# Kernel tuning notes

Hardware: AMD Instinct MI355X
Metric: run time of the kernel (lower is better)

The kernel has to match this reference:

```python
import jax, jax.numpy as jnp
import numpy as np

NUM_HEADS = 16


def setup_inputs() -> dict:
    key = jax.random.key(0)
    ks = jax.random.split(key, 5)
    B, N, C = 4, 2048, 1024
    x = jax.random.normal(ks[0], (B, N, C), dtype=jnp.float32)
    mask = jax.random.randint(ks[1], (B, N), 0, 2, dtype=jnp.int32)
    W_qkv = jax.random.normal(ks[2], (C, 3 * C), dtype=jnp.float32) * (C ** -0.5)
    W_proj = jax.random.normal(ks[3], (C, C), dtype=jnp.float32) * (C ** -0.5)
    b_proj = jnp.zeros((C,), dtype=jnp.float32)
    return {"x": x, "mask": mask, "W_qkv": W_qkv, "W_proj": W_proj, "b_proj": b_proj}


def reference(x, mask, W_qkv, W_proj, b_proj):
    B, N, C = x.shape
    H = NUM_HEADS
    hd = C // H
    scale = hd ** -0.5
    # qkv projection -> [3, B, H, N, hd]
    qkv = (x @ W_qkv).reshape(B, N, 3, H, hd).transpose(2, 0, 3, 1, 4)
    q, k, v = qkv[0], qkv[1], qkv[2]
    attn = jnp.einsum('bhqd,bhkd->bhqk', q, k) * scale  # [B,H,N,N]
    add_mask = (mask[:, None, None, :] != 1).astype(jnp.float32) * -10000.0
    attn = jax.nn.softmax(attn + add_mask, axis=-1)
    out = jnp.einsum('bhqk,bhkd->bhqd', attn, v)  # [B,H,N,hd]
    out = out.transpose(0, 2, 1, 3).reshape(B, N, C)
    return out @ W_proj + b_proj
```

## Files before the change

### kernel.cpp

```cpp
#include <hip/hip_runtime.h>

typedef unsigned short u16;
typedef unsigned int u32;
typedef unsigned long long u64;
typedef __attribute__((ext_vector_type(8))) short short8;
typedef __attribute__((ext_vector_type(4))) float f32x4;

#define QSCALE 0.18033688f

__device__ __forceinline__ u16 f2bf(float f) {
  u32 u = __builtin_bit_cast(u32, f);
  u += 0x7fffu + ((u >> 16) & 1u);
  return (u16)(u >> 16);
}

__device__ __forceinline__ float fexp2(float x) {
#if __has_builtin(__builtin_amdgcn_exp2f)
  return __builtin_amdgcn_exp2f(x);
#else
  return exp2f(x);
#endif
}

__device__ __forceinline__ void glds16(u16* lds, const u16* g) {
  __builtin_amdgcn_global_load_lds(
      (const __attribute__((address_space(1))) u32*)g,
      (__attribute__((address_space(3))) u32*)lds, 16, 0, 0);
}

#define MFMA(a, b, c) __builtin_amdgcn_mfma_f32_16x16x32_bf16((a), (b), (c), 0, 0, 0)


__global__ __launch_bounds__(256) void prep(const float* __restrict__ x,
                                            const int* __restrict__ mask,
                                            const float* __restrict__ Wqkv,
                                            const float* __restrict__ Wproj,
                                            u16* __restrict__ xb,
                                            u16* __restrict__ wqkvt,
                                            u16* __restrict__ wprojt,
                                            int* __restrict__ s2t,
                                            int* __restrict__ nkbuf) {
  __shared__ float tile[64][65];
  __shared__ int wtot[4];
  __shared__ int wbase[5];
  const int bid = blockIdx.x, t = threadIdx.x;

  if (bid < 8192) {
    int i = bid * 256 + t;
    float4 v = ((const float4*)x)[i];
    union { u16 s[4]; u64 ll; } u;
    u.s[0] = f2bf(v.x); u.s[1] = f2bf(v.y); u.s[2] = f2bf(v.z); u.s[3] = f2bf(v.w);
    ((u64*)xb)[i] = u.ll;
    return;
  }
  if (bid < 9216) {
    const float* Wm; u16* Wt; int Cc, bj, bi;
    if (bid < 8960) { int tt = bid - 8192; Wm = Wqkv;  Wt = wqkvt;  Cc = 3072; bj = tt % 48; bi = tt / 48; }
    else            { int tt = bid - 8960; Wm = Wproj; Wt = wprojt; Cc = 1024; bj = tt & 15; bi = tt >> 4; }
    const int r = t >> 4, c4 = (t & 15) << 2;
    for (int rr = r; rr < 64; rr += 16) {
      float4 v = *(const float4*)&Wm[(size_t)(bi * 64 + rr) * Cc + bj * 64 + c4];
      tile[rr][c4] = v.x; tile[rr][c4 + 1] = v.y; tile[rr][c4 + 2] = v.z; tile[rr][c4 + 3] = v.w;
    }
    __syncthreads();
    for (int rr = r; rr < 64; rr += 16) {
      union { u16 s[4]; u64 ll; } u;
      u.s[0] = f2bf(tile[c4][rr]);
      u.s[1] = f2bf(tile[c4 + 1][rr]);
      u.s[2] = f2bf(tile[c4 + 2][rr]);
      u.s[3] = f2bf(tile[c4 + 3][rr]);
      *(u64*)&Wt[(size_t)(bj * 64 + rr) * 1024 + bi * 64 + c4] = u.ll;
    }
    return;
  }
  const int b = bid - 9216;
  const int lane = t & 63, w = t >> 6;
  int m8[8], c = 0;
  #pragma unroll
  for (int j = 0; j < 8; j++) {
    m8[j] = (mask[b * 2048 + t * 8 + j] == 1);
    c += m8[j];
  }
  int incl = c;
  #pragma unroll
  for (int off = 1; off < 64; off <<= 1) {
    int v = __shfl_up(incl, off);
    if (lane >= off) incl += v;
  }
  if (lane == 63) wtot[w] = incl;
  __syncthreads();
  if (t == 0) {
    int s = 0;
    for (int i = 0; i < 4; i++) { wbase[i] = s; s += wtot[i]; }
    wbase[4] = s;
  }
  __syncthreads();
  const int nk = wbase[4];
  int urun = wbase[w] + incl - c;
  #pragma unroll
  for (int j = 0; j < 8; j++) {
    int tok = t * 8 + j;
    int slot = m8[j] ? urun : nk + (tok - urun);
    s2t[b * 2048 + slot] = b * 2048 + tok;
    urun += m8[j];
  }
  if (t == 0) nkbuf[b] = nk;
}

__global__ __launch_bounds__(256, 4) void gemm_fused(const u16* __restrict__ xb,
                                                     const u16* __restrict__ wqkvt,
                                                     const int* __restrict__ s2t,
                                                     const int* __restrict__ nkbuf,
                                                     u16* __restrict__ qbuf,
                                                     u16* __restrict__ kc,
                                                     u16* __restrict__ vtc) {
  __shared__ u16 Asm[128 * 64];
  __shared__ u16 Bsm[128 * 64];
  const int bid = blockIdx.x;
  const int role = bid >> 9;
  const int sub = bid & 511;
  const int tid = threadIdx.x, lane = tid & 63, w = tid >> 6;
  const int quad = lane >> 4, l15 = lane & 15;
  const int wm = (w >> 1) * 64, wn = (w & 1) * 64;
  const int srow = lane >> 3;
  const int gcc = ((lane & 7) ^ srow) * 8;
  const int rx8 = (l15 & 7);

  int m0, n0;
  if (role == 2) { m0 = (sub >> 6) * 128; n0 = (sub & 63) * 128; }
  else           { m0 = (sub & 63) * 128; n0 = (sub >> 6) * 128; }
  if (role == 1 && (m0 & 2047) >= nkbuf[m0 >> 11]) return;
  if (role == 2 && (n0 & 2047) >= nkbuf[n0 >> 11]) return;

  int arow[4], brow[4];
  #pragma unroll
  for (int c = 0; c < 4; ++c) {
    int rit = (w * 4 + c) * 8 + srow;
    if (role == 0)      { arow[c] = m0 + rit;            brow[c] = n0 + rit; }
    else if (role == 1) { arow[c] = s2t[m0 + rit];       brow[c] = 1024 + n0 + rit; }
    else                { arow[c] = 2048 + m0 + rit;     brow[c] = s2t[n0 + rit]; }
  }
  const u16 *Asrc = (role == 2) ? wqkvt : xb;
  const u16 *Bsrc = (role == 2) ? xb : wqkvt;

  f32x4 acc[4][4];
  #pragma unroll
  for (int i = 0; i < 4; i++)
    #pragma unroll
    for (int j = 0; j < 4; j++)
      #pragma unroll
      for (int r = 0; r < 4; r++) acc[i][j][r] = 0.f;

  for (int kt = 0; kt < 1024; kt += 64) {
    __syncthreads();
    #pragma unroll
    for (int c = 0; c < 4; ++c) {
      int chunk = w * 4 + c;
      glds16(&Asm[chunk * 512], &Asrc[(size_t)arow[c] * 1024 + kt + gcc]);
      glds16(&Bsm[chunk * 512], &Bsrc[(size_t)brow[c] * 1024 + kt + gcc]);
    }
    __syncthreads();
    #pragma unroll
    for (int ks = 0; ks < 2; ++ks) {
      int pc = ((ks * 4 + quad) ^ rx8) * 8;
      short8 av[4], bv[4];
      #pragma unroll
      for (int i = 0; i < 4; i++)
        av[i] = *(const short8*)&Asm[(wm + i * 16 + l15) * 64 + pc];
      #pragma unroll
      for (int j = 0; j < 4; j++)
        bv[j] = *(const short8*)&Bsm[(wn + j * 16 + l15) * 64 + pc];
      #pragma unroll
      for (int i = 0; i < 4; i++)
        #pragma unroll
        for (int j = 0; j < 4; j++)
          acc[i][j] = MFMA(av[i], bv[j], acc[i][j]);
    }
  }

  if (role == 2) {
    #pragma unroll
    for (int j = 0; j < 4; j++) {
      int col = n0 + wn + j * 16 + l15;
      int bb = col >> 11, sl = col & 2047;
      #pragma unroll
      for (int i = 0; i < 4; i++)
        #pragma unroll
        for (int r = 0; r < 4; r++) {
          int row = m0 + wm + i * 16 + quad * 4 + r;
          vtc[(size_t)(bb * 1024 + row) * 2048 + sl] = f2bf(acc[i][j][r]);
        }
    }
  } else {
    u16* dst = (role == 0) ? qbuf : kc;
    const float sc = (role == 0) ? QSCALE : 1.f;
    #pragma unroll
    for (int i = 0; i < 4; i++)
      #pragma unroll
      for (int j = 0; j < 4; j++) {
        int col = n0 + wn + j * 16 + l15;
        #pragma unroll
        for (int r = 0; r < 4; r++) {
          int row = m0 + wm + i * 16 + quad * 4 + r;
          dst[(size_t)row * 1024 + col] = f2bf(acc[i][j][r] * sc);
        }
      }
  }
}

__global__ __launch_bounds__(256, 2) void attn_kernel(const u16* __restrict__ q,
                                                      const u16* __restrict__ kc,
                                                      const u16* __restrict__ vtc,
                                                      const int* __restrict__ nkbuf,
                                                      u16* __restrict__ ao) {
  __shared__ u16 Ksm[2][2][64 * 64];
  __shared__ u16 Vsm[2][2][64 * 64];
  const int h = blockIdx.x, b = blockIdx.y, qt = blockIdx.z;
  const int tid = threadIdx.x, lane = tid & 63, w = tid >> 6;
  const int quad = lane >> 4, l15 = lane & 15;
  const int q0 = qt * 256 + w * 64;
  const int srow = lane >> 3;
  const int gcc = ((lane & 7) ^ srow) * 8;
  const int rx8 = (l15 & 7);
  const int nk = nkbuf[b];
  const int nt2 = (nk + 127) >> 7;
  const int quad8 = quad * 8;

  int vrow[2], prow[2];
  #pragma unroll
  for (int c = 0; c < 2; ++c) {
    int row = (w * 2 + c) * 8 + srow;
    vrow[c] = row;
    prow[c] = ((row >> 4) & 1) * 32 + ((row >> 2) & 3) * 8 + ((row >> 5) & 1) * 4 + (row & 3);
  }

  short8 ones;
  #pragma unroll
  for (int z = 0; z < 8; z++) ones[z] = (short)0x3F80;

  short8 qf[4][2];
  #pragma unroll
  for (int i = 0; i < 4; i++)
    #pragma unroll
    for (int ks = 0; ks < 2; ks++)
      qf[i][ks] = *(const short8*)&q[(size_t)(b * 2048 + q0 + i * 16 + l15) * 1024 +
                                     h * 64 + ks * 32 + quad * 8];

  f32x4 o[4][4], osum[4];
  #pragma unroll
  for (int i = 0; i < 4; i++) {
    #pragma unroll
    for (int r = 0; r < 4; r++) osum[i][r] = 0.f;
    #pragma unroll
    for (int jd = 0; jd < 4; jd++)
      #pragma unroll
      for (int r = 0; r < 4; r++) o[i][jd][r] = 0.f;
  }

#define STAGEKV(pb_, t_) {                                                             \
    const int k0s = (t_) * 128;                                                        \
    _Pragma("unroll") for (int c = 0; c < 2; ++c) {                                    \
      int chunk = w * 2 + c;                                                           \
      glds16(&Ksm[pb_][0][chunk * 512],                                                \
             &kc[(size_t)(b * 2048 + k0s + prow[c]) * 1024 + h * 64 + gcc]);           \
      glds16(&Vsm[pb_][0][chunk * 512],                                                \
             &vtc[(size_t)(b * 1024 + h * 64 + vrow[c]) * 2048 + k0s + gcc]);          \
      glds16(&Ksm[pb_][1][chunk * 512],                                                \
             &kc[(size_t)(b * 2048 + k0s + 64 + prow[c]) * 1024 + h * 64 + gcc]);      \
      glds16(&Vsm[pb_][1][chunk * 512],                                                \
             &vtc[(size_t)(b * 1024 + h * 64 + vrow[c]) * 2048 + k0s + 64 + gcc]);     \
    }                                                                                  \
  }

#define SUBTILE(pb_, st_, kbase_)                                                      \
  {                                                                                    \
    f32x4 s[4][4];                                                                     \
    _Pragma("unroll") for (int j = 0; j < 4; j++)                                      \
      _Pragma("unroll") for (int i = 0; i < 4; i++)                                    \
        _Pragma("unroll") for (int r = 0; r < 4; r++) s[j][i][r] = 0.f;                \
    _Pragma("unroll") for (int ks = 0; ks < 2; ks++) {                                 \
      int pc = ((ks * 4 + quad) ^ rx8) * 8;                                            \
      short8 kf[4];                                                                    \
      _Pragma("unroll") for (int j = 0; j < 4; j++)                                    \
        kf[j] = *(const short8*)&Ksm[pb_][st_][(j * 16 + l15) * 64 + pc];              \
      __builtin_amdgcn_s_setprio(1);                                                   \
      _Pragma("unroll") for (int j = 0; j < 4; j++)                                    \
        _Pragma("unroll") for (int i = 0; i < 4; i++)                                  \
          s[j][i] = MFMA(kf[j], qf[i][ks], s[j][i]);                                   \
      __builtin_amdgcn_s_setprio(0);                                                   \
    }                                                                                  \
    const bool tail = ((kbase_) + 64 > nk);                                            \
    short8 pf[4][2];                                                                   \
    _Pragma("unroll") for (int i = 0; i < 4; i++) {                                    \
      float p[4][4];                                                                   \
      if (!tail) {                                                                     \
        _Pragma("unroll") for (int j = 0; j < 4; j++)                                  \
          _Pragma("unroll") for (int r = 0; r < 4; r++)                                \
            p[j][r] = fexp2(s[j][i][r]);                                               \
      } else {                                                                         \
        _Pragma("unroll") for (int j = 0; j < 4; j++)                                  \
          _Pragma("unroll") for (int r = 0; r < 4; r++) {                              \
            int slot = (kbase_) + (j & 1) * 32 + quad8 + (j >> 1) * 4 + r;             \
            float e = fexp2(s[j][i][r]);                                               \
            p[j][r] = (slot < nk) ? e : 0.f;                                           \
          }                                                                            \
      }                                                                                \
      _Pragma("unroll") for (int ks = 0; ks < 2; ks++) {                               \
        union { u32 u[4]; short8 v; } pk;                                              \
        u32 a0 = __builtin_bit_cast(u32, p[ks][0]) + 0x8000u;                          \
        u32 a1 = __builtin_bit_cast(u32, p[ks][1]) + 0x8000u;                          \
        u32 a2 = __builtin_bit_cast(u32, p[ks][2]) + 0x8000u;                          \
        u32 a3 = __builtin_bit_cast(u32, p[ks][3]) + 0x8000u;                          \
        u32 b0 = __builtin_bit_cast(u32, p[ks + 2][0]) + 0x8000u;                      \
        u32 b1 = __builtin_bit_cast(u32, p[ks + 2][1]) + 0x8000u;                      \
        u32 b2 = __builtin_bit_cast(u32, p[ks + 2][2]) + 0x8000u;                      \
        u32 b3 = __builtin_bit_cast(u32, p[ks + 2][3]) + 0x8000u;                      \
        pk.u[0] = __builtin_amdgcn_perm(a1, a0, 0x07060302u);                          \
        pk.u[1] = __builtin_amdgcn_perm(a3, a2, 0x07060302u);                          \
        pk.u[2] = __builtin_amdgcn_perm(b1, b0, 0x07060302u);                          \
        pk.u[3] = __builtin_amdgcn_perm(b3, b2, 0x07060302u);                          \
        pf[i][ks] = pk.v;                                                              \
      }                                                                                \
    }                                                                                  \
    _Pragma("unroll") for (int ks = 0; ks < 2; ks++) {                                 \
      int pcv = ((ks * 4 + quad) ^ rx8) * 8;                                           \
      short8 vf[4];                                                                    \
      _Pragma("unroll") for (int jd = 0; jd < 4; jd++)                                 \
        vf[jd] = *(const short8*)&Vsm[pb_][st_][(jd * 16 + l15) * 64 + pcv];           \
      __builtin_amdgcn_s_setprio(1);                                                   \
      _Pragma("unroll") for (int i = 0; i < 4; i++) {                                  \
        osum[i] = MFMA(pf[i][ks], ones, osum[i]);                                      \
        _Pragma("unroll") for (int jd = 0; jd < 4; jd++)                               \
          o[i][jd] = MFMA(pf[i][ks], vf[jd], o[i][jd]);                                \
      }                                                                                \
      __builtin_amdgcn_s_setprio(0);                                                   \
    }                                                                                  \
  }

  STAGEKV(0, 0)
  __syncthreads();
  for (int t = 0; t < nt2; ++t) {
    const int k0 = t * 128;
    const int pb = t & 1;
    if (t + 1 < nt2) STAGEKV(pb ^ 1, t + 1)
    SUBTILE(pb, 0, k0)
    if (k0 + 64 < nk) SUBTILE(pb, 1, k0 + 64)
    __syncthreads();
  }
#undef SUBTILE
#undef STAGEKV

  #pragma unroll
  for (int i = 0; i < 4; i++)
    #pragma unroll
    for (int r = 0; r < 4; r++) {
      float inv = 1.f / osum[i][r];
      size_t row = (size_t)(b * 2048 + q0 + i * 16 + quad * 4 + r);
      #pragma unroll
      for (int jd = 0; jd < 4; jd++)
        ao[row * 1024 + h * 64 + jd * 16 + l15] = f2bf(o[i][jd][r] * inv);
    }
}

__global__ __launch_bounds__(256, 3) void gemm_proj(const u16* __restrict__ A,
                                                    const u16* __restrict__ Bt,
                                                    const float* __restrict__ bias,
                                                    float* __restrict__ out) {
  __shared__ u16 Asm[2][128 * 64];
  __shared__ u16 Bsm[2][128 * 64];
  const int tid = threadIdx.x, lane = tid & 63, w = tid >> 6;
  const int quad = lane >> 4, l15 = lane & 15;
  const int m0 = (blockIdx.x & 63) * 128, n0 = (blockIdx.x >> 6) * 128;
  const int wm = (w >> 1) * 64, wn = (w & 1) * 64;
  const int srow = lane >> 3;
  const int gcc = ((lane & 7) ^ srow) * 8;
  const int rx8 = (l15 & 7);
  f32x4 acc[4][4];
  #pragma unroll
  for (int i = 0; i < 4; i++)
    #pragma unroll
    for (int j = 0; j < 4; j++)
      #pragma unroll
      for (int r = 0; r < 4; r++) acc[i][j][r] = 0.f;

#define STAGEP(pb_, kt_) {                                                             \
    _Pragma("unroll") for (int c = 0; c < 4; ++c) {                                    \
      int chunk = w * 4 + c;                                                           \
      int row = chunk * 8 + srow;                                                      \
      glds16(&Asm[pb_][chunk * 512], &A[(size_t)(m0 + row) * 1024 + (kt_) + gcc]);     \
      glds16(&Bsm[pb_][chunk * 512], &Bt[(size_t)(n0 + row) * 1024 + (kt_) + gcc]);    \
    }                                                                                  \
  }

  STAGEP(0, 0)
  __syncthreads();
  for (int kt = 0, t = 0; kt < 1024; kt += 64, ++t) {
    const int pb = t & 1;
    if (kt + 64 < 1024) STAGEP(pb ^ 1, kt + 64)
    #pragma unroll
    for (int ks = 0; ks < 2; ++ks) {
      int pc = ((ks * 4 + quad) ^ rx8) * 8;
      short8 av[4], bv[4];
      #pragma unroll
      for (int i = 0; i < 4; i++)
        av[i] = *(const short8*)&Asm[pb][(wm + i * 16 + l15) * 64 + pc];
      #pragma unroll
      for (int j = 0; j < 4; j++)
        bv[j] = *(const short8*)&Bsm[pb][(wn + j * 16 + l15) * 64 + pc];
      #pragma unroll
      for (int i = 0; i < 4; i++)
        #pragma unroll
        for (int j = 0; j < 4; j++)
          acc[i][j] = MFMA(av[i], bv[j], acc[i][j]);
    }
    __syncthreads();
  }
#undef STAGEP

  #pragma unroll
  for (int j = 0; j < 4; j++) {
    int col = n0 + wn + j * 16 + l15;
    float bj = bias[col];
    #pragma unroll
    for (int i = 0; i < 4; i++) {
      #pragma unroll
      for (int r = 0; r < 4; r++) {
        int row = m0 + wm + i * 16 + quad * 4 + r;
        out[(size_t)row * 1024 + col] = acc[i][j][r] + bj;
      }
    }
  }
}

extern "C" void kernel_launch(void* const* d_in, const int* in_sizes, int n_in,
                              void* d_out, int out_size, void* d_ws, size_t ws_size,
                              hipStream_t stream) {
  (void)in_sizes; (void)n_in; (void)out_size; (void)ws_size;
  const float* x     = (const float*)d_in[0];
  const int*   mask  = (const int*)d_in[1];
  const float* Wqkv  = (const float*)d_in[2];
  const float* Wproj = (const float*)d_in[3];
  const float* bproj = (const float*)d_in[4];
  float* out = (float*)d_out;
  char* ws = (char*)d_ws;

  size_t off = 0;
  u16* xb     = (u16*)(ws + off); off += 8192ull * 1024 * 2;
  u16* wqkvt  = (u16*)(ws + off); off += 3072ull * 1024 * 2;
  u16* wprojt = (u16*)(ws + off); off += 1024ull * 1024 * 2;
  u16* qbuf   = (u16*)(ws + off); off += 8192ull * 1024 * 2;
  u16* kcbuf  = (u16*)(ws + off); off += 4096ull * 2048 * 2;
  u16* vtcbuf = (u16*)(ws + off); off += 4096ull * 2048 * 2;
  int* s2t    = (int*)(ws + off); off += 8192ull * 4;
  int* nkbuf  = (int*)(ws + off); off += 4 * 4;
  u16* aobuf  = xb;

  prep<<<9220, 256, 0, stream>>>(x, mask, Wqkv, Wproj, xb, wqkvt, wprojt, s2t, nkbuf);
  gemm_fused<<<1536, 256, 0, stream>>>(xb, wqkvt, s2t, nkbuf, qbuf, kcbuf, vtcbuf);
  attn_kernel<<<dim3(16, 4, 8), 256, 0, stream>>>(qbuf, kcbuf, vtcbuf, nkbuf, aobuf);
  gemm_proj<<<512, 256, 0, stream>>>(aobuf, wprojt, bproj, out);
}
```

Before: 206.4 us.

## Rewrite QKV GEMM as 256x256 tile with double-buffered LDS pipeline

The fused QKV projection GEMM moves from 128x128 tiles with 4 waves to 256x256 tiles with 8 waves. It uses double-buffered LDS, staging the next K-tile's A and B loads interleaved with MFMA phases, and adds raw s_barrier plus s_setprio around the MFMA bursts. The aim is to raise operand reuse per LDS byte and hide global-to-LDS latency behind compute, replacing the old load-sync-compute loop. The costs are 128KB of LDS per block, a larger accumulator register footprint, and coarser early-exit granularity for the masked K/V roles.

```diff
diff --git a/kernel.cpp b/kernel.cpp
--- a/kernel.cpp
+++ b/kernel.cpp
@@ -29,6 +29,7 @@
 }
 
 #define MFMA(a, b, c) __builtin_amdgcn_mfma_f32_16x16x32_bf16((a), (b), (c), 0, 0, 0)
+#define SBAR() asm volatile("s_barrier" ::: "memory")
 
 
 __global__ __launch_bounds__(256) void prep(const float* __restrict__ x,
@@ -107,102 +108,138 @@
   if (t == 0) nkbuf[b] = nk;
 }
 
-__global__ __launch_bounds__(256, 4) void gemm_fused(const u16* __restrict__ xb,
+__global__ __launch_bounds__(512, 2) void gemm_fused(const u16* __restrict__ xb,
                                                      const u16* __restrict__ wqkvt,
                                                      const int* __restrict__ s2t,
                                                      const int* __restrict__ nkbuf,
                                                      u16* __restrict__ qbuf,
                                                      u16* __restrict__ kc,
                                                      u16* __restrict__ vtc) {
-  __shared__ u16 Asm[128 * 64];
-  __shared__ u16 Bsm[128 * 64];
+  __shared__ u16 ldsf[2 * 32768];
   const int bid = blockIdx.x;
-  const int role = bid >> 9;
-  const int sub = bid & 511;
+  const int role = bid >> 7;
+  const int sub = bid & 127;
   const int tid = threadIdx.x, lane = tid & 63, w = tid >> 6;
   const int quad = lane >> 4, l15 = lane & 15;
-  const int wm = (w >> 1) * 64, wn = (w & 1) * 64;
-  const int srow = lane >> 3;
-  const int gcc = ((lane & 7) ^ srow) * 8;
-  const int rx8 = (l15 & 7);
+  const int wm = (w >> 2) * 128, wn = (w & 3) * 64;
+  const int rx8 = l15 & 7;
+  const int srow6 = tid >> 3;
+  const int sgc = ((tid & 7) ^ (srow6 & 7)) * 8;
 
   int m0, n0;
-  if (role == 2) { m0 = (sub >> 6) * 128; n0 = (sub & 63) * 128; }
-  else           { m0 = (sub & 63) * 128; n0 = (sub >> 6) * 128; }
+  if (role == 2) { m0 = (sub >> 5) * 256; n0 = (sub & 31) * 256; }
+  else           { m0 = (sub & 31) * 256; n0 = (sub >> 5) * 256; }
   if (role == 1 && (m0 & 2047) >= nkbuf[m0 >> 11]) return;
   if (role == 2 && (n0 & 2047) >= nkbuf[n0 >> 11]) return;
 
-  int arow[4], brow[4];
-  #pragma unroll
-  for (int c = 0; c < 4; ++c) {
-    int rit = (w * 4 + c) * 8 + srow;
-    if (role == 0)      { arow[c] = m0 + rit;            brow[c] = n0 + rit; }
-    else if (role == 1) { arow[c] = s2t[m0 + rit];       brow[c] = 1024 + n0 + rit; }
-    else                { arow[c] = 2048 + m0 + rit;     brow[c] = s2t[n0 + rit]; }
-  }
-  const u16 *Asrc = (role == 2) ? wqkvt : xb;
-  const u16 *Bsrc = (role == 2) ? xb : wqkvt;
-
-  f32x4 acc[4][4];
-  #pragma unroll
-  for (int i = 0; i < 4; i++)
+  int aro[4], bro[4];
+  #pragma unroll
+  for (int q = 0; q < 4; ++q) {
+    int r = q * 64 + srow6;
+    if (role == 0)      { aro[q] = m0 + r;         bro[q] = n0 + r; }
+    else if (role == 1) { aro[q] = s2t[m0 + r];    bro[q] = 1024 + n0 + r; }
+    else                { aro[q] = 2048 + m0 + r;  bro[q] = s2t[n0 + r]; }
+  }
+  const u16* Asrc = (role == 2) ? wqkvt : xb;
+  const u16* Bsrc = (role == 2) ? xb : wqkvt;
+
+#define ABUF(T) (ldsf + (((T) & 1) * 32768))
+#define BBUF(T) (ldsf + (((T) & 1) * 32768 + 16384))
+#define STG_A(H, T) { \
+  glds16(ABUF(T) + ((H) * 128 + w * 8) * 64,      &Asrc[(size_t)aro[(H) * 2]     * 1024 + (T) * 64 + sgc]); \
+  glds16(ABUF(T) + ((H) * 128 + 64 + w * 8) * 64, &Asrc[(size_t)aro[(H) * 2 + 1] * 1024 + (T) * 64 + sgc]); }
+#define STG_B(H, T) { \
+  glds16(BBUF(T) + ((H) * 128 + w * 8) * 64,      &Bsrc[(size_t)bro[(H) * 2]     * 1024 + (T) * 64 + sgc]); \
+  glds16(BBUF(T) + ((H) * 128 + 64 + w * 8) * 64, &Bsrc[(size_t)bro[(H) * 2 + 1] * 1024 + (T) * 64 + sgc]); }
+
+#define LDA8(MH) \
+  _Pragma("unroll") for (int ii = 0; ii < 4; ++ii) \
+    _Pragma("unroll") for (int ks = 0; ks < 2; ++ks) \
+      av[ii][ks] = *(const short8*)&LA[(wm + (MH) * 64 + ii * 16 + l15) * 64 + (((ks * 4 + quad) ^ rx8) * 8)];
+#define LDB4(NH) \
+  _Pragma("unroll") for (int jj = 0; jj < 2; ++jj) \
+    _Pragma("unroll") for (int ks = 0; ks < 2; ++ks) \
+      bv[jj][ks] = *(const short8*)&LB[(wn + (NH) * 32 + jj * 16 + l15) * 64 + (((ks * 4 + quad) ^ rx8) * 8)];
+#define MM16(MH, NH) \
+  __builtin_amdgcn_s_setprio(1); \
+  _Pragma("unroll") for (int ks = 0; ks < 2; ++ks) \
+    _Pragma("unroll") for (int ii = 0; ii < 4; ++ii) \
+      _Pragma("unroll") for (int jj = 0; jj < 2; ++jj) \
+        acc[(MH) * 4 + ii][(NH) * 2 + jj] = MFMA(av[ii][ks], bv[jj][ks], acc[(MH) * 4 + ii][(NH) * 2 + jj]); \
+  __builtin_amdgcn_s_setprio(0);
+
+  f32x4 acc[8][4];
+  #pragma unroll
+  for (int i = 0; i < 8; i++)
     #pragma unroll
     for (int j = 0; j < 4; j++)
       #pragma unroll
       for (int r = 0; r < 4; r++) acc[i][j][r] = 0.f;
 
-  for (int kt = 0; kt < 1024; kt += 64) {
-    __syncthreads();
-    #pragma unroll
-    for (int c = 0; c < 4; ++c) {
-      int chunk = w * 4 + c;
-      glds16(&Asm[chunk * 512], &Asrc[(size_t)arow[c] * 1024 + kt + gcc]);
-      glds16(&Bsm[chunk * 512], &Bsrc[(size_t)brow[c] * 1024 + kt + gcc]);
-    }
-    __syncthreads();
-    #pragma unroll
-    for (int ks = 0; ks < 2; ++ks) {
-      int pc = ((ks * 4 + quad) ^ rx8) * 8;
-      short8 av[4], bv[4];
-      #pragma unroll
-      for (int i = 0; i < 4; i++)
-        av[i] = *(const short8*)&Asm[(wm + i * 16 + l15) * 64 + pc];
-      #pragma unroll
-      for (int j = 0; j < 4; j++)
-        bv[j] = *(const short8*)&Bsm[(wn + j * 16 + l15) * 64 + pc];
-      #pragma unroll
-      for (int i = 0; i < 4; i++)
-        #pragma unroll
-        for (int j = 0; j < 4; j++)
-          acc[i][j] = MFMA(av[i], bv[j], acc[i][j]);
-    }
-  }
+  STG_A(0, 0) STG_A(1, 0) STG_B(0, 0) STG_B(1, 0)
+  STG_B(0, 1) STG_B(1, 1)
+  asm volatile("s_waitcnt vmcnt(4)" ::: "memory");
+  SBAR();
+
+  for (int T = 0; T < 16; ++T) {
+    const u16* LA = ABUF(T);
+    const u16* LB = BBUF(T);
+    short8 av[4][2], bv[2][2];
+    LDA8(0) LDB4(0)
+    if (T + 1 < 16) { STG_A(0, T + 1) }
+    SBAR();
+    MM16(0, 0)
+    SBAR();
+    LDA8(1)
+    if (T + 1 < 16) { STG_A(1, T + 1) }
+    SBAR();
+    MM16(1, 0)
+    SBAR();
+    LDB4(1)
+    SBAR();
+    MM16(1, 1)
+    SBAR();
+    LDA8(0)
+    if (T + 2 < 16) { STG_B(0, T + 2) STG_B(1, T + 2) }
+    SBAR();
+    MM16(0, 1)
+    if (T + 2 < 16)      { asm volatile("s_waitcnt vmcnt(4)" ::: "memory"); }
+    else if (T + 1 < 16) { asm volatile("s_waitcnt vmcnt(0)" ::: "memory"); }
+    SBAR();
+  }
+#undef ABUF
+#undef BBUF
+#undef STG_A
+#undef STG_B
+#undef LDA8
+#undef LDB4
+#undef MM16
 
   if (role == 2) {
     #pragma unroll
-    for (int j = 0; j < 4; j++) {
-      int col = n0 + wn + j * 16 + l15;
+    for (int nj = 0; nj < 4; nj++) {
+      int col = n0 + wn + nj * 16 + l15;
       int bb = col >> 11, sl = col & 2047;
       #pragma unroll
-      for (int i = 0; i < 4; i++)
+      for (int mi = 0; mi < 8; mi++)
         #pragma unroll
         for (int r = 0; r < 4; r++) {
-          int row = m0 + wm + i * 16 + quad * 4 + r;
-          vtc[(size_t)(bb * 1024 + row) * 2048 + sl] = f2bf(acc[i][j][r]);
+          int row = m0 + wm + mi * 16 + quad * 4 + r;
+          vtc[(size_t)(bb * 1024 + row) * 2048 + sl] = f2bf(acc[mi][nj][r]);
         }
     }
   } else {
     u16* dst = (role == 0) ? qbuf : kc;
     const float sc = (role == 0) ? QSCALE : 1.f;
     #pragma unroll
-    for (int i = 0; i < 4; i++)
-      #pragma unroll
-      for (int j = 0; j < 4; j++) {
-        int col = n0 + wn + j * 16 + l15;
+    for (int mi = 0; mi < 8; mi++)
+      #pragma unroll
+      for (int nj = 0; nj < 4; nj++) {
+        int col = n0 + wn + nj * 16 + l15;
         #pragma unroll
         for (int r = 0; r < 4; r++) {
-          int row = m0 + wm + i * 16 + quad * 4 + r;
-          dst[(size_t)row * 1024 + col] = f2bf(acc[i][j][r] * sc);
+          int row = m0 + wm + mi * 16 + quad * 4 + r;
+          dst[(size_t)row * 1024 + col] = f2bf(acc[mi][nj][r] * sc);
         }
       }
   }
@@ -456,7 +493,7 @@
   u16* aobuf  = xb;
 
   prep<<<9220, 256, 0, stream>>>(x, mask, Wqkv, Wproj, xb, wqkvt, wprojt, s2t, nkbuf);
-  gemm_fused<<<1536, 256, 0, stream>>>(xb, wqkvt, s2t, nkbuf, qbuf, kcbuf, vtcbuf);
+  gemm_fused<<<384, 512, 0, stream>>>(xb, wqkvt, s2t, nkbuf, qbuf, kcbuf, vtcbuf);
   attn_kernel<<<dim3(16, 4, 8), 256, 0, stream>>>(qbuf, kcbuf, vtcbuf, nkbuf, aobuf);
   gemm_proj<<<512, 256, 0, stream>>>(aobuf, wprojt, bproj, out);
 }
```

Measured after the change: 224.4 us. 1.09x slower.

## Double attention block to 8 waves sharing each staged K/V tile

Applied to the files above, without the earlier changes.

The attention kernel now uses 512 threads (8 waves) per block, with each block covering 512 query rows instead of 256, so the grid's z dimension halves. Each K/V tile staged in LDS is reused by twice as many waves, and each wave issues half as many global-to-LDS copies. The cost is half as many blocks (256), which may leave some of the GPU's compute units idle. Removing the min-blocks hint from launch bounds may also change register allocation and occupancy.

```diff
diff --git a/kernel.cpp b/kernel.cpp
--- a/kernel.cpp
+++ b/kernel.cpp
@@ -208,17 +208,17 @@
   }
 }
 
-__global__ __launch_bounds__(256, 2) void attn_kernel(const u16* __restrict__ q,
-                                                      const u16* __restrict__ kc,
-                                                      const u16* __restrict__ vtc,
-                                                      const int* __restrict__ nkbuf,
-                                                      u16* __restrict__ ao) {
+__global__ __launch_bounds__(512) void attn_kernel(const u16* __restrict__ q,
+                                                   const u16* __restrict__ kc,
+                                                   const u16* __restrict__ vtc,
+                                                   const int* __restrict__ nkbuf,
+                                                   u16* __restrict__ ao) {
   __shared__ u16 Ksm[2][2][64 * 64];
   __shared__ u16 Vsm[2][2][64 * 64];
   const int h = blockIdx.x, b = blockIdx.y, qt = blockIdx.z;
   const int tid = threadIdx.x, lane = tid & 63, w = tid >> 6;
   const int quad = lane >> 4, l15 = lane & 15;
-  const int q0 = qt * 256 + w * 64;
+  const int q0 = qt * 512 + w * 64;
   const int srow = lane >> 3;
   const int gcc = ((lane & 7) ^ srow) * 8;
   const int rx8 = (l15 & 7);
@@ -226,13 +226,10 @@
   const int nt2 = (nk + 127) >> 7;
   const int quad8 = quad * 8;
 
-  int vrow[2], prow[2];
-  #pragma unroll
-  for (int c = 0; c < 2; ++c) {
-    int row = (w * 2 + c) * 8 + srow;
-    vrow[c] = row;
-    prow[c] = ((row >> 4) & 1) * 32 + ((row >> 2) & 3) * 8 + ((row >> 5) & 1) * 4 + (row & 3);
-  }
+  const int strow = w * 8 + srow;
+  const int vrow = strow;
+  const int prow = ((strow >> 4) & 1) * 32 + ((strow >> 2) & 3) * 8 +
+                   ((strow >> 5) & 1) * 4 + (strow & 3);
 
   short8 ones;
   #pragma unroll
@@ -259,17 +256,14 @@
 
 #define STAGEKV(pb_, t_) {                                                             \
     const int k0s = (t_) * 128;                                                        \
-    _Pragma("unroll") for (int c = 0; c < 2; ++c) {                                    \
-      int chunk = w * 2 + c;                                                           \
-      glds16(&Ksm[pb_][0][chunk * 512],                                                \
-             &kc[(size_t)(b * 2048 + k0s + prow[c]) * 1024 + h * 64 + gcc]);           \
-      glds16(&Vsm[pb_][0][chunk * 512],                                                \
-             &vtc[(size_t)(b * 1024 + h * 64 + vrow[c]) * 2048 + k0s + gcc]);          \
-      glds16(&Ksm[pb_][1][chunk * 512],                                                \
-             &kc[(size_t)(b * 2048 + k0s + 64 + prow[c]) * 1024 + h * 64 + gcc]);      \
-      glds16(&Vsm[pb_][1][chunk * 512],                                                \
-             &vtc[(size_t)(b * 1024 + h * 64 + vrow[c]) * 2048 + k0s + 64 + gcc]);     \
-    }                                                                                  \
+    glds16(&Ksm[pb_][0][w * 512],                                                      \
+           &kc[(size_t)(b * 2048 + k0s + prow) * 1024 + h * 64 + gcc]);                \
+    glds16(&Vsm[pb_][0][w * 512],                                                      \
+           &vtc[(size_t)(b * 1024 + h * 64 + vrow) * 2048 + k0s + gcc]);               \
+    glds16(&Ksm[pb_][1][w * 512],                                                      \
+           &kc[(size_t)(b * 2048 + k0s + 64 + prow) * 1024 + h * 64 + gcc]);           \
+    glds16(&Vsm[pb_][1][w * 512],                                                      \
+           &vtc[(size_t)(b * 1024 + h * 64 + vrow) * 2048 + k0s + 64 + gcc]);          \
   }
 
 #define SUBTILE(pb_, st_, kbase_)                                                      \
@@ -457,6 +451,6 @@
 
   prep<<<9220, 256, 0, stream>>>(x, mask, Wqkv, Wproj, xb, wqkvt, wprojt, s2t, nkbuf);
   gemm_fused<<<1536, 256, 0, stream>>>(xb, wqkvt, s2t, nkbuf, qbuf, kcbuf, vtcbuf);
-  attn_kernel<<<dim3(16, 4, 8), 256, 0, stream>>>(qbuf, kcbuf, vtcbuf, nkbuf, aobuf);
+  attn_kernel<<<dim3(16, 4, 4), 512, 0, stream>>>(qbuf, kcbuf, vtcbuf, nkbuf, aobuf);
   gemm_proj<<<512, 256, 0, stream>>>(aobuf, wprojt, bproj, out);
 }
```

Measured after the change: 211.5 us. 2.5% more time.
